# Optimization experiments

Hardware: AMD Instinct MI355X
Metric: run time of the kernel (lower is better)

The kernel has to match this reference:

```python
import jax, jax.numpy as jnp
import numpy as np

B, S, D_MODEL = 2, 2048, 2048
N_HEADS, N_KV_HEADS = 32, 8
HEAD_DIM = D_MODEL // N_HEADS  # 64


def setup_inputs() -> dict:
    key = jax.random.key(0)
    ks = jax.random.split(key, 7)
    # rope frequencies (as in standard RoPE; values just need to be the right shape)
    inv_freq = 1.0 / (10000.0 ** (jnp.arange(0, HEAD_DIM, 2, dtype=jnp.float32) / HEAD_DIM))
    t = jnp.arange(S, dtype=jnp.float32)
    freqs = t[:, None] * inv_freq[None, :]  # (S, head_dim//2)
    scale = 0.02
    return {
        "x": jax.random.normal(ks[0], (B, S, D_MODEL), jnp.float32),
        "cos": jnp.cos(freqs),
        "sin": jnp.sin(freqs),
        "Wq": jax.random.normal(ks[1], (N_HEADS * HEAD_DIM, D_MODEL), jnp.float32) * scale,
        "Wk": jax.random.normal(ks[2], (N_KV_HEADS * HEAD_DIM, D_MODEL), jnp.float32) * scale,
        "Wv": jax.random.normal(ks[3], (N_KV_HEADS * HEAD_DIM, D_MODEL), jnp.float32) * scale,
        "Wo": jax.random.normal(ks[4], (D_MODEL, D_MODEL), jnp.float32) * scale,
    }


def _apply_rope(x, cos, sin):
    # x: (B, H, S, D); cos/sin: (S, D//2)
    d = x.shape[-1]
    x1, x2 = x[..., : d // 2], x[..., d // 2:]
    c = cos[None, None]
    s = sin[None, None]
    return jnp.concatenate([x1 * c - x2 * s, x1 * s + x2 * c], axis=-1)


def reference(x, cos, sin, Wq, Wk, Wv, Wo):
    b, s, _ = x.shape
    hd = 2 * cos.shape[-1]
    h = Wq.shape[0] // hd
    kv = Wk.shape[0] // hd
    g = h // kv  # query heads per kv head

    q = (x @ Wq.T).reshape(b, s, h, hd).transpose(0, 2, 1, 3)    # (b,h,s,d)
    k = (x @ Wk.T).reshape(b, s, kv, hd).transpose(0, 2, 1, 3)   # (b,kv,s,d)
    v = (x @ Wv.T).reshape(b, s, kv, hd).transpose(0, 2, 1, 3)

    q = _apply_rope(q, cos, sin)
    k = _apply_rope(k, cos, sin)

    # GQA: group query heads instead of materializing repeated K/V
    qg = q.reshape(b, kv, g, s, hd)
    scale = 1.0 / jnp.sqrt(jnp.asarray(hd, x.dtype))
    scores = jnp.einsum('bkgsd,bktd->bkgst', qg, k) * scale      # (b,kv,g,s,s)
    causal = jnp.arange(s)[:, None] >= jnp.arange(s)[None, :]
    scores = jnp.where(causal[None, None, None], scores, jnp.asarray(-jnp.inf, scores.dtype))
    attn = jax.nn.softmax(scores, axis=-1)
    out = jnp.einsum('bkgst,bktd->bkgsd', attn, v)               # (b,kv,g,s,d)
    out = out.reshape(b, h, s, hd).transpose(0, 2, 1, 3).reshape(b, s, h * hd)
    return out @ Wo.T
```

## Files before the change

kernel.cpp:

```cpp
#include <hip/hip_runtime.h>
#include <hip/hip_bf16.h>

typedef __bf16 bf16;
typedef __attribute__((ext_vector_type(8))) __bf16 bf16x8;
typedef __attribute__((ext_vector_type(4))) __bf16 bf16x4;
typedef __attribute__((ext_vector_type(4))) float f32x4;

#define B_SZ 2
#define S_SZ 2048
#define D_SZ 2048
#define H_SZ 32
#define KV_SZ 8
#define HD_SZ 64
#define M_SZ (B_SZ * S_SZ)
#define NQKV 3072

#define GLDS(g, s) __builtin_amdgcn_global_load_lds( \
    (const __attribute__((address_space(1))) void*)(g), \
    (__attribute__((address_space(3))) void*)(s), 16, 0, 0)

__global__ void cvt_f32_bf16(const float* __restrict__ in, bf16* __restrict__ out, int n4) {
    int i = blockIdx.x * blockDim.x + threadIdx.x;
    if (i >= n4) return;
    float4 v = ((const float4*)in)[i];
    bf16x4 o;
    o.x = (bf16)v.x; o.y = (bf16)v.y; o.z = (bf16)v.z; o.w = (bf16)v.w;
    ((bf16x4*)out)[i] = o;
}

__global__ void cvt_w_qkv(const float* __restrict__ Wq, const float* __restrict__ Wk,
                          const float* __restrict__ Wv, bf16* __restrict__ Wf,
                          int n1, int n2) {
    int i = blockIdx.x * blockDim.x + threadIdx.x;
    if (i >= n1 + 2 * n2) return;
    const float* src;
    int off;
    if (i < n1)            { src = Wq; off = i; }
    else if (i < n1 + n2)  { src = Wk; off = i - n1; }
    else                   { src = Wv; off = i - n1 - n2; }
    float4 v = ((const float4*)src)[off];
    bf16x4 o;
    o.x = (bf16)v.x; o.y = (bf16)v.y; o.z = (bf16)v.z; o.w = (bf16)v.w;
    ((bf16x4*)Wf)[i] = o;
}

#define BK 32

__global__ __launch_bounds__(256)
void gemm_qkv(const bf16* __restrict__ A, const bf16* __restrict__ Bw,
              bf16* __restrict__ Qb, bf16* __restrict__ Kb, bf16* __restrict__ Vtb,
              const float* __restrict__ cosp, const float* __restrict__ sinp,
              float qscale)
{
    const int K = D_SZ;
    __shared__ __align__(16) bf16 As[128 * BK];
    __shared__ __align__(16) bf16 Bs[128 * BK];
    const int tid  = threadIdx.x;
    const int lane = tid & 63;
    const int wave = tid >> 6;
    const int waveM = wave >> 1, waveN = wave & 1;
    const int c = lane & 15, quad = lane >> 4;
    const int rowBase = blockIdx.y * 128;
    const int colBase = blockIdx.x * 128;

    const int is0 = wave * 2, is1 = wave * 2 + 1;
    const int rr   = lane >> 2;
    const int kOff = (lane & 3) * 8;

    const bf16* Ag0 = A  + (size_t)(rowBase + is0 * 16 + rr) * K + kOff;
    const bf16* Ag1 = A  + (size_t)(rowBase + is1 * 16 + rr) * K + kOff;
    const bf16* Bg0 = Bw + (size_t)(colBase + is0 * 16 + rr) * K + kOff;
    const bf16* Bg1 = Bw + (size_t)(colBase + is1 * 16 + rr) * K + kOff;

    bf16* sA0 = As + is0 * 512;
    bf16* sA1 = As + is1 * 512;
    bf16* sB0 = Bs + is0 * 512;
    bf16* sB1 = Bs + is1 * 512;

    f32x4 acc[4][4] = {};

    for (int k0 = 0; k0 < K; k0 += BK) {
        GLDS(Ag0 + k0, sA0);
        GLDS(Ag1 + k0, sA1);
        GLDS(Bg0 + k0, sB0);
        GLDS(Bg1 + k0, sB1);
        __syncthreads();

        bf16x8 af[4], bfr[4];
#pragma unroll
        for (int mi = 0; mi < 4; mi++)
            af[mi] = *(const bf16x8*)(As + (waveM * 64 + mi * 16 + c) * BK + quad * 8);
#pragma unroll
        for (int ni = 0; ni < 4; ni++)
            bfr[ni] = *(const bf16x8*)(Bs + (waveN * 64 + ni * 16 + c) * BK + quad * 8);
#pragma unroll
        for (int mi = 0; mi < 4; mi++)
#pragma unroll
            for (int ni = 0; ni < 4; ni++)
                acc[mi][ni] = __builtin_amdgcn_mfma_f32_16x16x32_bf16(af[mi], bfr[ni], acc[mi][ni], 0, 0, 0);
        __syncthreads();
    }

    const int mBase = rowBase + waveM * 64;
    const int nBase = colBase + waveN * 64;

    if (nBase < 2560) {
        bf16* dst; int hh, Hn; float sc;
        if (nBase < 2048) { dst = Qb; hh = nBase >> 6;        Hn = H_SZ;  sc = qscale; }
        else              { dst = Kb; hh = (nBase >> 6) - 32; Hn = KV_SZ; sc = 1.0f;  }
#pragma unroll
        for (int mi = 0; mi < 4; mi++) {
#pragma unroll
            for (int r = 0; r < 4; r++) {
                int row = mBase + mi * 16 + quad * 4 + r;
                int b = row >> 11;
                int s = row & 2047;
                const float* cr = cosp + (size_t)s * 32;
                const float* sr = sinp + (size_t)s * 32;
                size_t base = ((size_t)(b * Hn + hh) * S_SZ + s) * 64;
#pragma unroll
                for (int ni = 0; ni < 2; ni++) {
                    int d = ni * 16 + c;
                    float x1 = acc[mi][ni][r];
                    float x2 = acc[mi][ni + 2][r];
                    float cv = cr[d], sv = sr[d];
                    dst[base + d]      = (bf16)((x1 * cv - x2 * sv) * sc);
                    dst[base + d + 32] = (bf16)((x1 * sv + x2 * cv) * sc);
                }
            }
        }
    } else {
        const int kvh = (nBase >> 6) - 40;
        const int b   = mBase >> 11;
        const int s0  = mBase & 2047;
#pragma unroll
        for (int ni = 0; ni < 4; ni++) {
            int d = ni * 16 + c;
            size_t base = ((size_t)(b * KV_SZ + kvh) * 64 + d) * (size_t)S_SZ;
#pragma unroll
            for (int mi = 0; mi < 4; mi++) {
                int s = s0 + mi * 16 + quad * 4;
#pragma unroll
                for (int r = 0; r < 4; r++)
                    Vtb[base + s + r] = (bf16)acc[mi][ni][r];
            }
        }
    }
}

__global__ __launch_bounds__(256)
void gemm_out(const bf16* __restrict__ A, const bf16* __restrict__ Bw,
              float* __restrict__ Co, int N, int K)
{
    __shared__ __align__(16) bf16 As[128 * BK];
    __shared__ __align__(16) bf16 Bs[128 * BK];
    const int tid  = threadIdx.x;
    const int lane = tid & 63;
    const int wave = tid >> 6;
    const int waveM = wave >> 1, waveN = wave & 1;
    const int c = lane & 15, quad = lane >> 4;
    const int rowBase = blockIdx.y * 128;
    const int colBase = blockIdx.x * 128;

    const int is0 = wave * 2, is1 = wave * 2 + 1;
    const int rr   = lane >> 2;
    const int kOff = (lane & 3) * 8;

    const bf16* Ag0 = A  + (size_t)(rowBase + is0 * 16 + rr) * K + kOff;
    const bf16* Ag1 = A  + (size_t)(rowBase + is1 * 16 + rr) * K + kOff;
    const bf16* Bg0 = Bw + (size_t)(colBase + is0 * 16 + rr) * K + kOff;
    const bf16* Bg1 = Bw + (size_t)(colBase + is1 * 16 + rr) * K + kOff;

    bf16* sA0 = As + is0 * 512;
    bf16* sA1 = As + is1 * 512;
    bf16* sB0 = Bs + is0 * 512;
    bf16* sB1 = Bs + is1 * 512;

    f32x4 acc[4][4] = {};

    for (int k0 = 0; k0 < K; k0 += BK) {
        GLDS(Ag0 + k0, sA0);
        GLDS(Ag1 + k0, sA1);
        GLDS(Bg0 + k0, sB0);
        GLDS(Bg1 + k0, sB1);
        __syncthreads();

        bf16x8 af[4], bfr[4];
#pragma unroll
        for (int mi = 0; mi < 4; mi++)
            af[mi] = *(const bf16x8*)(As + (waveM * 64 + mi * 16 + c) * BK + quad * 8);
#pragma unroll
        for (int ni = 0; ni < 4; ni++)
            bfr[ni] = *(const bf16x8*)(Bs + (waveN * 64 + ni * 16 + c) * BK + quad * 8);
#pragma unroll
        for (int mi = 0; mi < 4; mi++)
#pragma unroll
            for (int ni = 0; ni < 4; ni++)
                acc[mi][ni] = __builtin_amdgcn_mfma_f32_16x16x32_bf16(af[mi], bfr[ni], acc[mi][ni], 0, 0, 0);
        __syncthreads();
    }

    const int mBase = rowBase + waveM * 64;
    const int nBase = colBase + waveN * 64;
#pragma unroll
    for (int mi = 0; mi < 4; mi++)
#pragma unroll
        for (int ni = 0; ni < 4; ni++) {
            int col = nBase + ni * 16 + c;
#pragma unroll
            for (int r = 0; r < 4; r++) {
                int row = mBase + mi * 16 + quad * 4 + r;
                Co[(size_t)row * N + col] = acc[mi][ni][r];
            }
        }
}

#define LDF 72

__global__ __launch_bounds__(256, 2)
void flash_attn(const bf16* __restrict__ Q, const bf16* __restrict__ Kc,
                const bf16* __restrict__ Vt, bf16* __restrict__ Aout, int bh0)
{
    __shared__ __align__(16) bf16 Ks[64 * LDF];
    __shared__ __align__(16) bf16 Vs[64 * LDF];
    __shared__ __align__(16) bf16 Ps[4 * 16 * LDF];

    const int tid  = threadIdx.x;
    const int lane = tid & 63;
    const int wave = tid >> 6;
    const int c = lane & 15, quad = lane >> 4;
    const int qloc = wave * 16 + c;

    const int i  = blockIdx.x;
    const int tA = 31 - i, tB = i;
    const int q0A = tA << 6, q0B = tB << 6;

    const int bh = blockIdx.y + bh0;
    const int b  = bh >> 5;
    const int h  = bh & 31;
    const int kv = h >> 2;

    const bf16* Qp = Q  + (size_t)bh * (S_SZ * 64);
    const bf16* Kp = Kc + (size_t)(b * KV_SZ + kv) * (S_SZ * 64);
    const bf16* Vp = Vt + (size_t)(b * KV_SZ + kv) * (64 * S_SZ);

    bf16x8 aqA[2], aqB[2];
    {
        const bf16* qa = Qp + (size_t)(q0A + qloc) * 64 + quad * 8;
        aqA[0] = *(const bf16x8*)qa;  aqA[1] = *(const bf16x8*)(qa + 32);
        const bf16* qb = Qp + (size_t)(q0B + qloc) * 64 + quad * 8;
        aqB[0] = *(const bf16x8*)qb;  aqB[1] = *(const bf16x8*)(qb + 32);
    }

    f32x4 oA[4] = {}, oB[4] = {};
    f32x4 lA = {}, lB = {};

    bf16x8 ones;
#pragma unroll
    for (int j = 0; j < 8; j++) ones[j] = (bf16)1.0f;

    const int srow = tid >> 3;
    const int soff = (tid & 7) * 8;
    const bf16* Kg0 = Kp + (size_t)srow * 64 + soff;
    const bf16* Kg1 = Kp + (size_t)(srow + 32) * 64 + soff;
    const bf16* Vg0 = Vp + (size_t)srow * S_SZ + soff;
    const bf16* Vg1 = Vp + (size_t)(srow + 32) * S_SZ + soff;

    uint4 pk0 = *(const uint4*)Kg0, pk1 = *(const uint4*)Kg1;
    uint4 pv0 = *(const uint4*)Vg0, pv1 = *(const uint4*)Vg1;

    bf16* Pw = Ps + wave * 16 * LDF;

    for (int kt = 0; kt <= tA; kt++) {
        *(uint4*)(Ks + srow * LDF + soff)        = pk0;
        *(uint4*)(Ks + (srow + 32) * LDF + soff) = pk1;
        *(uint4*)(Vs + srow * LDF + soff)        = pv0;
        *(uint4*)(Vs + (srow + 32) * LDF + soff) = pv1;
        __syncthreads();
        if (kt < tA) {
            pk0 = *(const uint4*)(Kg0 + (size_t)(kt + 1) * 4096);
            pk1 = *(const uint4*)(Kg1 + (size_t)(kt + 1) * 4096);
            pv0 = *(const uint4*)(Vg0 + (kt + 1) * 64);
            pv1 = *(const uint4*)(Vg1 + (kt + 1) * 64);
        }

        bf16x8 ak[2][4], av[2][4];
#pragma unroll
        for (int ks = 0; ks < 2; ks++)
#pragma unroll
            for (int ni = 0; ni < 4; ni++) {
                ak[ks][ni] = *(const bf16x8*)(Ks + (ni * 16 + c) * LDF + ks * 32 + quad * 8);
                av[ks][ni] = *(const bf16x8*)(Vs + (ni * 16 + c) * LDF + ks * 32 + quad * 8);
            }

        const bool diagA = (kt == tA);
        const bool doB   = (kt <= tB);
        const bool diagB = (kt == tB);

        {
            f32x4 sc[4] = {};
#pragma unroll
            for (int ks = 0; ks < 2; ks++)
#pragma unroll
                for (int ni = 0; ni < 4; ni++)
                    sc[ni] = __builtin_amdgcn_mfma_f32_16x16x32_bf16(ak[ks][ni], aqA[ks], sc[ni], 0, 0, 0);
#pragma unroll
            for (int ni = 0; ni < 4; ni++) {
                bf16x4 pk;
#pragma unroll
                for (int r = 0; r < 4; r++) {
                    float p = exp2f(sc[ni][r]);
                    if (diagA && (ni * 16 + quad * 4 + r) > qloc) p = 0.f;
                    pk[r] = (bf16)p;
                }
                *(bf16x4*)(Pw + c * LDF + ni * 16 + quad * 4) = pk;
            }
#pragma unroll
            for (int ks = 0; ks < 2; ks++) {
                bf16x8 bp = *(const bf16x8*)(Pw + c * LDF + ks * 32 + quad * 8);
                lA = __builtin_amdgcn_mfma_f32_16x16x32_bf16(ones, bp, lA, 0, 0, 0);
#pragma unroll
                for (int ni = 0; ni < 4; ni++)
                    oA[ni] = __builtin_amdgcn_mfma_f32_16x16x32_bf16(av[ks][ni], bp, oA[ni], 0, 0, 0);
            }
        }
        if (doB) {
            f32x4 sc[4] = {};
#pragma unroll
            for (int ks = 0; ks < 2; ks++)
#pragma unroll
                for (int ni = 0; ni < 4; ni++)
                    sc[ni] = __builtin_amdgcn_mfma_f32_16x16x32_bf16(ak[ks][ni], aqB[ks], sc[ni], 0, 0, 0);
#pragma unroll
            for (int ni = 0; ni < 4; ni++) {
                bf16x4 pk;
#pragma unroll
                for (int r = 0; r < 4; r++) {
                    float p = exp2f(sc[ni][r]);
                    if (diagB && (ni * 16 + quad * 4 + r) > qloc) p = 0.f;
                    pk[r] = (bf16)p;
                }
                *(bf16x4*)(Pw + c * LDF + ni * 16 + quad * 4) = pk;
            }
#pragma unroll
            for (int ks = 0; ks < 2; ks++) {
                bf16x8 bp = *(const bf16x8*)(Pw + c * LDF + ks * 32 + quad * 8);
                lB = __builtin_amdgcn_mfma_f32_16x16x32_bf16(ones, bp, lB, 0, 0, 0);
#pragma unroll
                for (int ni = 0; ni < 4; ni++)
                    oB[ni] = __builtin_amdgcn_mfma_f32_16x16x32_bf16(av[ks][ni], bp, oB[ni], 0, 0, 0);
            }
        }
        __syncthreads();
    }

    {
        float ila = 1.f / lA[0];
        float ilb = 1.f / lB[0];
        bf16* pa = Aout + ((size_t)(b * S_SZ + q0A + qloc)) * D_SZ + h * 64;
        bf16* pb = Aout + ((size_t)(b * S_SZ + q0B + qloc)) * D_SZ + h * 64;
#pragma unroll
        for (int ni = 0; ni < 4; ni++) {
            bf16x4 wa, wb;
#pragma unroll
            for (int r = 0; r < 4; r++) {
                wa[r] = (bf16)(oA[ni][r] * ila);
                wb[r] = (bf16)(oB[ni][r] * ilb);
            }
            *(bf16x4*)(pa + ni * 16 + quad * 4) = wa;
            *(bf16x4*)(pb + ni * 16 + quad * 4) = wb;
        }
    }
}

extern "C" void kernel_launch(void* const* d_in, const int* in_sizes, int n_in,
                              void* d_out, int out_size, void* d_ws, size_t ws_size,
                              hipStream_t stream) {
    const float* x    = (const float*)d_in[0];
    const float* cosp = (const float*)d_in[1];
    const float* sinp = (const float*)d_in[2];
    const float* Wq   = (const float*)d_in[3];
    const float* Wk   = (const float*)d_in[4];
    const float* Wv   = (const float*)d_in[5];
    const float* Wo   = (const float*)d_in[6];
    float* out = (float*)d_out;

    const int M = M_SZ;
    const int D = D_SZ;
    const int NKV = KV_SZ * HD_SZ;

    bf16* xb   = (bf16*)d_ws;
    bf16* Wf   = xb  + (size_t)M * D;
    bf16* Qb   = Wf  + (size_t)NQKV * D;
    bf16* Kb   = Qb  + (size_t)M * D;
    bf16* Vtb  = Kb  + (size_t)B_SZ * KV_SZ * S_SZ * 64;
    bf16* attn = xb;
    bf16* wob  = Wf;

    const int n1 = D * D / 4, n2 = NKV * D / 4;

    cvt_f32_bf16<<<(M * D / 4 + 255) / 256, 256, 0, stream>>>(x, xb, M * D / 4);
    cvt_w_qkv<<<(n1 + 2 * n2 + 255) / 256, 256, 0, stream>>>(Wq, Wk, Wv, Wf, n1, n2);

    const float qscale = 0.125f * 1.44269504089f;

    gemm_qkv<<<dim3(NQKV / 128, M / 128), 256, 0, stream>>>(xb, Wf, Qb, Kb, Vtb, cosp, sinp, qscale);

    cvt_f32_bf16<<<(D * D / 4 + 255) / 256, 256, 0, stream>>>(Wo, wob, D * D / 4);

    flash_attn<<<dim3(16, 32), 256, 0, stream>>>(Qb, Kb, Vtb, attn, 0);
    flash_attn<<<dim3(16, 32), 256, 0, stream>>>(Qb, Kb, Vtb, attn, 32);

    gemm_out<<<dim3(D / 128, M / 128), 256, 0, stream>>>(attn, wob, out, D, D);
}
```

Measured before the change: 341.9 us.

## Double GEMM K-tile with XOR-swizzled LDS, merge conversions and attention launches

Both GEMMs now stage K-tiles of 64 instead of 32, using an XOR-swizzled shared-memory layout to avoid bank conflicts on fragment reads. Each tile runs two MFMA sub-steps, so barriers and loop overhead are halved. The x and QKV weight conversions are fused into one kernel, and the two flash-attention launches are merged into a single grid covering all batch-heads. Shared memory per GEMM block doubles, which may lower occupancy.

New measurement: 313.2 us. 1.09x faster.

```diff
diff --git a/kernel.cpp b/kernel.cpp
--- a/kernel.cpp
+++ b/kernel.cpp
@@ -19,6 +19,26 @@
     (const __attribute__((address_space(1))) void*)(g), \
     (__attribute__((address_space(3))) void*)(s), 16, 0, 0)
 
+__global__ void cvt_all(const float* __restrict__ x, const float* __restrict__ Wq,
+                        const float* __restrict__ Wk, const float* __restrict__ Wv,
+                        bf16* __restrict__ xb, bf16* __restrict__ Wf,
+                        int nx, int n1, int n2) {
+    int i = blockIdx.x * blockDim.x + threadIdx.x;
+    const float* src; bf16* dst; int off;
+    if (i < nx)                { src = x;  dst = xb; off = i; }
+    else {
+        int j = i - nx;
+        if (j < n1)            { src = Wq; dst = Wf; off = j; }
+        else if (j < n1 + n2)  { src = Wk; dst = Wf + (size_t)4 * n1; off = j - n1; }
+        else if (j < n1+2*n2)  { src = Wv; dst = Wf + (size_t)4 * (n1 + n2); off = j - n1 - n2; }
+        else return;
+    }
+    float4 v = ((const float4*)src)[off];
+    bf16x4 o;
+    o.x = (bf16)v.x; o.y = (bf16)v.y; o.z = (bf16)v.z; o.w = (bf16)v.w;
+    ((bf16x4*)dst)[off] = o;
+}
+
 __global__ void cvt_f32_bf16(const float* __restrict__ in, bf16* __restrict__ out, int n4) {
     int i = blockIdx.x * blockDim.x + threadIdx.x;
     if (i >= n4) return;
@@ -28,23 +48,42 @@
     ((bf16x4*)out)[i] = o;
 }
 
-__global__ void cvt_w_qkv(const float* __restrict__ Wq, const float* __restrict__ Wk,
-                          const float* __restrict__ Wv, bf16* __restrict__ Wf,
-                          int n1, int n2) {
-    int i = blockIdx.x * blockDim.x + threadIdx.x;
-    if (i >= n1 + 2 * n2) return;
-    const float* src;
-    int off;
-    if (i < n1)            { src = Wq; off = i; }
-    else if (i < n1 + n2)  { src = Wk; off = i - n1; }
-    else                   { src = Wv; off = i - n1 - n2; }
-    float4 v = ((const float4*)src)[off];
-    bf16x4 o;
-    o.x = (bf16)v.x; o.y = (bf16)v.y; o.z = (bf16)v.z; o.w = (bf16)v.w;
-    ((bf16x4*)Wf)[i] = o;
-}
-
-#define BK 32
+#define BK 64
+
+#define GEMM_CORE(A_, B_, Kdim)                                                  \
+    const int g8 = lane >> 3;                                                    \
+    const int chs = ((lane & 7) ^ g8) * 8;                                       \
+    const bf16* Ag = A_ + (size_t)(rowBase + g8) * Kdim + chs;                   \
+    const bf16* Bg = B_ + (size_t)(colBase + g8) * Kdim + chs;                   \
+    f32x4 acc[4][4] = {};                                                        \
+    for (int k0 = 0; k0 < Kdim; k0 += BK) {                                      \
+        _Pragma("unroll")                                                        \
+        for (int j = 0; j < 4; j++) {                                            \
+            int is = wave * 4 + j;                                               \
+            GLDS(Ag + (size_t)(is * 8) * Kdim + k0, As + is * 512);              \
+            GLDS(Bg + (size_t)(is * 8) * Kdim + k0, Bs + is * 512);              \
+        }                                                                        \
+        __syncthreads();                                                         \
+        _Pragma("unroll")                                                        \
+        for (int ks = 0; ks < 2; ks++) {                                         \
+            bf16x8 af[4], bfr[4];                                                \
+            _Pragma("unroll")                                                    \
+            for (int mi = 0; mi < 4; mi++)                                       \
+                af[mi] = *(const bf16x8*)(As + (waveM * 64 + mi * 16 + c) * 64   \
+                                          + (((ks << 2) + quad) ^ (c & 7)) * 8); \
+            _Pragma("unroll")                                                    \
+            for (int ni = 0; ni < 4; ni++)                                       \
+                bfr[ni] = *(const bf16x8*)(Bs + (waveN * 64 + ni * 16 + c) * 64  \
+                                          + (((ks << 2) + quad) ^ (c & 7)) * 8); \
+            _Pragma("unroll")                                                    \
+            for (int mi = 0; mi < 4; mi++)                                       \
+                _Pragma("unroll")                                                \
+                for (int ni = 0; ni < 4; ni++)                                   \
+                    acc[mi][ni] = __builtin_amdgcn_mfma_f32_16x16x32_bf16(       \
+                        af[mi], bfr[ni], acc[mi][ni], 0, 0, 0);                  \
+        }                                                                        \
+        __syncthreads();                                                         \
+    }
 
 __global__ __launch_bounds__(256)
 void gemm_qkv(const bf16* __restrict__ A, const bf16* __restrict__ Bw,
@@ -52,7 +91,6 @@
               const float* __restrict__ cosp, const float* __restrict__ sinp,
               float qscale)
 {
-    const int K = D_SZ;
     __shared__ __align__(16) bf16 As[128 * BK];
     __shared__ __align__(16) bf16 Bs[128 * BK];
     const int tid  = threadIdx.x;
@@ -63,43 +101,7 @@
     const int rowBase = blockIdx.y * 128;
     const int colBase = blockIdx.x * 128;
 
-    const int is0 = wave * 2, is1 = wave * 2 + 1;
-    const int rr   = lane >> 2;
-    const int kOff = (lane & 3) * 8;
-
-    const bf16* Ag0 = A  + (size_t)(rowBase + is0 * 16 + rr) * K + kOff;
-    const bf16* Ag1 = A  + (size_t)(rowBase + is1 * 16 + rr) * K + kOff;
-    const bf16* Bg0 = Bw + (size_t)(colBase + is0 * 16 + rr) * K + kOff;
-    const bf16* Bg1 = Bw + (size_t)(colBase + is1 * 16 + rr) * K + kOff;
-
-    bf16* sA0 = As + is0 * 512;
-    bf16* sA1 = As + is1 * 512;
-    bf16* sB0 = Bs + is0 * 512;
-    bf16* sB1 = Bs + is1 * 512;
-
-    f32x4 acc[4][4] = {};
-
-    for (int k0 = 0; k0 < K; k0 += BK) {
-        GLDS(Ag0 + k0, sA0);
-        GLDS(Ag1 + k0, sA1);
-        GLDS(Bg0 + k0, sB0);
-        GLDS(Bg1 + k0, sB1);
-        __syncthreads();
-
-        bf16x8 af[4], bfr[4];
-#pragma unroll
-        for (int mi = 0; mi < 4; mi++)
-            af[mi] = *(const bf16x8*)(As + (waveM * 64 + mi * 16 + c) * BK + quad * 8);
-#pragma unroll
-        for (int ni = 0; ni < 4; ni++)
-            bfr[ni] = *(const bf16x8*)(Bs + (waveN * 64 + ni * 16 + c) * BK + quad * 8);
-#pragma unroll
-        for (int mi = 0; mi < 4; mi++)
-#pragma unroll
-            for (int ni = 0; ni < 4; ni++)
-                acc[mi][ni] = __builtin_amdgcn_mfma_f32_16x16x32_bf16(af[mi], bfr[ni], acc[mi][ni], 0, 0, 0);
-        __syncthreads();
-    }
+    GEMM_CORE(A, Bw, D_SZ)
 
     const int mBase = rowBase + waveM * 64;
     const int nBase = colBase + waveN * 64;
@@ -162,43 +164,7 @@
     const int rowBase = blockIdx.y * 128;
     const int colBase = blockIdx.x * 128;
 
-    const int is0 = wave * 2, is1 = wave * 2 + 1;
-    const int rr   = lane >> 2;
-    const int kOff = (lane & 3) * 8;
-
-    const bf16* Ag0 = A  + (size_t)(rowBase + is0 * 16 + rr) * K + kOff;
-    const bf16* Ag1 = A  + (size_t)(rowBase + is1 * 16 + rr) * K + kOff;
-    const bf16* Bg0 = Bw + (size_t)(colBase + is0 * 16 + rr) * K + kOff;
-    const bf16* Bg1 = Bw + (size_t)(colBase + is1 * 16 + rr) * K + kOff;
-
-    bf16* sA0 = As + is0 * 512;
-    bf16* sA1 = As + is1 * 512;
-    bf16* sB0 = Bs + is0 * 512;
-    bf16* sB1 = Bs + is1 * 512;
-
-    f32x4 acc[4][4] = {};
-
-    for (int k0 = 0; k0 < K; k0 += BK) {
-        GLDS(Ag0 + k0, sA0);
-        GLDS(Ag1 + k0, sA1);
-        GLDS(Bg0 + k0, sB0);
-        GLDS(Bg1 + k0, sB1);
-        __syncthreads();
-
-        bf16x8 af[4], bfr[4];
-#pragma unroll
-        for (int mi = 0; mi < 4; mi++)
-            af[mi] = *(const bf16x8*)(As + (waveM * 64 + mi * 16 + c) * BK + quad * 8);
-#pragma unroll
-        for (int ni = 0; ni < 4; ni++)
-            bfr[ni] = *(const bf16x8*)(Bs + (waveN * 64 + ni * 16 + c) * BK + quad * 8);
-#pragma unroll
-        for (int mi = 0; mi < 4; mi++)
-#pragma unroll
-            for (int ni = 0; ni < 4; ni++)
-                acc[mi][ni] = __builtin_amdgcn_mfma_f32_16x16x32_bf16(af[mi], bfr[ni], acc[mi][ni], 0, 0, 0);
-        __syncthreads();
-    }
+    GEMM_CORE(A, Bw, K)
 
     const int mBase = rowBase + waveM * 64;
     const int nBase = colBase + waveN * 64;
@@ -219,7 +185,7 @@
 
 __global__ __launch_bounds__(256, 2)
 void flash_attn(const bf16* __restrict__ Q, const bf16* __restrict__ Kc,
-                const bf16* __restrict__ Vt, bf16* __restrict__ Aout, int bh0)
+                const bf16* __restrict__ Vt, bf16* __restrict__ Aout)
 {
     __shared__ __align__(16) bf16 Ks[64 * LDF];
     __shared__ __align__(16) bf16 Vs[64 * LDF];
@@ -235,7 +201,7 @@
     const int tA = 31 - i, tB = i;
     const int q0A = tA << 6, q0B = tB << 6;
 
-    const int bh = blockIdx.y + bh0;
+    const int bh = blockIdx.y;
     const int b  = bh >> 5;
     const int h  = bh & 31;
     const int kv = h >> 2;
@@ -397,19 +363,17 @@
     bf16* attn = xb;
     bf16* wob  = Wf;
 
-    const int n1 = D * D / 4, n2 = NKV * D / 4;
-
-    cvt_f32_bf16<<<(M * D / 4 + 255) / 256, 256, 0, stream>>>(x, xb, M * D / 4);
-    cvt_w_qkv<<<(n1 + 2 * n2 + 255) / 256, 256, 0, stream>>>(Wq, Wk, Wv, Wf, n1, n2);
+    const int nx = M * D / 4, n1 = D * D / 4, n2 = NKV * D / 4;
+
+    cvt_all<<<(nx + n1 + 2 * n2 + 255) / 256, 256, 0, stream>>>(x, Wq, Wk, Wv, xb, Wf, nx, n1, n2);
 
     const float qscale = 0.125f * 1.44269504089f;
 
     gemm_qkv<<<dim3(NQKV / 128, M / 128), 256, 0, stream>>>(xb, Wf, Qb, Kb, Vtb, cosp, sinp, qscale);
 
-    cvt_f32_bf16<<<(D * D / 4 + 255) / 256, 256, 0, stream>>>(Wo, wob, D * D / 4);
-
-    flash_attn<<<dim3(16, 32), 256, 0, stream>>>(Qb, Kb, Vtb, attn, 0);
-    flash_attn<<<dim3(16, 32), 256, 0, stream>>>(Qb, Kb, Vtb, attn, 32);
+    cvt_f32_bf16<<<(n1 + 255) / 256, 256, 0, stream>>>(Wo, wob, n1);
+
+    flash_attn<<<dim3(16, B_SZ * H_SZ), 256, 0, stream>>>(Qb, Kb, Vtb, attn);
 
     gemm_out<<<dim3(D / 128, M / 128), 256, 0, stream>>>(attn, wob, out, D, D);
 }
```
